# Performance work log

Hardware: AMD Instinct MI355X
Metric: run time of the kernel (lower is better)

## Reference

```python
import jax, jax.numpy as jnp
import numpy as np

# Config (mirrors HymbaLayer init + env constants)
DIM = 1024; NH = 16; NKV = 4; D = 64          # head_dim = DIM // NH
NATTN = NH // 2; NSSM = NH // 2; KVREP = NATTN // NKV
S = 16          # _HYMBA_SSM_STATE
NMETA = 4       # _HYMBA_META_TOK
BASE = 10000.0  # rope_base
CHUNK = 64      # _HYMBA_SCAN_CHUNK
B, T = 2, 2048


def _rms_norm(x, eps=1e-6):
    return x * jax.lax.rsqrt(jnp.mean(x * x, -1, keepdims=True) + eps)


def _rotary_cs(t_len, d, base):
    inv = 1.0 / (base ** (jnp.arange(0, d, 2, dtype=jnp.float32) / d))  # (d/2,)
    f = jnp.arange(t_len, dtype=jnp.float32)[:, None] * inv[None, :]    # (T, d/2)
    return jnp.cos(f), jnp.sin(f)


def _apply_rot(x, cos, sin):
    # x: (B, H, T, D); rotate-half style rotary
    d2 = x.shape[-1] // 2
    x1, x2 = x[..., :d2], x[..., d2:]
    c, s = cos[None, None], sin[None, None]
    return jnp.concatenate([x1 * c - x2 * s, x1 * s + x2 * c], -1)


def _scan_chunks(log_a, u, chunk):
    # Exact chunk-parallel diagonal scan: h_t = exp(log_a_t)*h_{t-1} + u_t
    b, t, s = u.shape
    nc = t // chunk
    la = log_a.reshape(b, nc, chunk, s)
    uu = u.reshape(b, nc, chunk, s)
    log_p = jnp.clip(jnp.cumsum(la, axis=2), -30.0, 0.0)
    p = jnp.exp(log_p)
    h_local = p * jnp.cumsum(uu * jnp.exp(-log_p), axis=2)

    def step(h0, args):
        hl, pc = args                          # (B, chunk, S)
        hc = hl + pc * h0[:, None, :]
        return hc[:, -1], hc

    _, hs = jax.lax.scan(step, jnp.zeros((b, s), u.dtype),
                         (jnp.swapaxes(h_local, 0, 1), jnp.swapaxes(p, 0, 1)))
    return jnp.swapaxes(hs, 0, 1).reshape(b, t, s)


def _mamba_head(logA, Bw, Cw, dtw, dtb, Ow, x):
    # x: (B, T, D); selective SSM with diagonal A
    dt = jnp.minimum(jax.nn.softplus(x @ dtw.T + dtb), 1.0)   # (B,T,S)
    A = jnp.minimum(-jnp.exp(logA), 10.0)                      # (S,)
    log_a = jnp.clip(dt * A, -0.5, 0.0)
    Bx = (x @ Bw.T) * dt
    Cc = x @ Cw.T
    h = _scan_chunks(log_a, Bx, CHUNK)                         # (B,T,S)
    y = jnp.sum(Cc * h, -1, keepdims=True)
    return h @ Ow.T + y * x[..., :1]


def _forward(x, meta_tokens, c_q_w, c_k_w, c_v_w, q_gain, ssm_in_w, proj_w,
             attn_scale, ssm_scale, ssm_logA, ssm_Bw, ssm_Cw, ssm_dtw, ssm_dtb, ssm_Ow):
    b, t, c = x.shape
    x_ext = jnp.concatenate([jnp.broadcast_to(meta_tokens, (b, NMETA, c)), x], 1)
    t_ext = t + NMETA
    q = (x_ext @ c_q_w.T).reshape(b, t_ext, NH, D).transpose(0, 2, 1, 3)
    k = (x_ext @ c_k_w.T).reshape(b, t_ext, NKV, D).transpose(0, 2, 1, 3)
    v = (x_ext @ c_v_w.T).reshape(b, t_ext, NKV, D).transpose(0, 2, 1, 3)
    q = _rms_norm(q); k = _rms_norm(k)
    cos, sin = _rotary_cs(t_ext, D, BASE)
    q = _apply_rot(q, cos, sin); k = _apply_rot(k, cos, sin)
    # GQA attention over the first NATTN heads, causal over T_ext
    q_attn = q[:, :NATTN] * q_gain[None, :, None, None]
    k_exp = jnp.repeat(k, KVREP, axis=1)
    v_exp = jnp.repeat(v, KVREP, axis=1)
    scores = jnp.einsum('bhqd,bhkd->bhqk', q_attn, k_exp) / jnp.sqrt(jnp.float32(D))
    mask = jnp.tril(jnp.ones((t_ext, t_ext), bool))
    scores = jnp.where(mask[None, None], scores, -jnp.inf)
    attn = jax.nn.softmax(scores, axis=-1)
    ao = jnp.einsum('bhqk,bhkd->bhqd', attn, v_exp)
    ao = ao[:, :, NMETA:].transpose(0, 2, 1, 3).reshape(b, t, NATTN * D) * attn_scale
    # SSM branch on the original (un-prepended) tokens
    ssm_x = (x @ ssm_in_w.T).reshape(b, t, NSSM, D)
    ssm_out = jax.vmap(_mamba_head, in_axes=(0, 0, 0, 0, 0, 0, 2), out_axes=2)(
        ssm_logA, ssm_Bw, ssm_Cw, ssm_dtw, ssm_dtb, ssm_Ow, ssm_x)
    ssm_out = ssm_out.reshape(b, t, NSSM * D) * ssm_scale
    return jnp.concatenate([ao, ssm_out], -1) @ proj_w.T


def setup_inputs() -> dict:
    key = jax.random.key(0)
    ks = jax.random.split(key, 16)
    r = lambda k, sh, sc=0.02: jax.random.normal(k, sh, jnp.float32) * sc
    return {
        'x': jax.random.normal(ks[0], (B, T, DIM), jnp.float32),
        'meta_tokens': r(ks[1], (1, NMETA, DIM)),
        'c_q_w': r(ks[2], (DIM, DIM)),
        'c_k_w': r(ks[3], (NKV * D, DIM)),
        'c_v_w': r(ks[4], (NKV * D, DIM)),
        'q_gain': jnp.full((NATTN,), 1.0, jnp.float32),
        'ssm_in_w': r(ks[5], (NSSM * D, DIM)),
        'proj_w': r(ks[6], (DIM, DIM)),
        'attn_scale': jnp.ones((1,), jnp.float32),
        'ssm_scale': jnp.ones((1,), jnp.float32),
        'ssm_logA': jax.random.normal(ks[7], (NSSM, S), jnp.float32) * 0.5,
        'ssm_Bw': r(ks[8], (NSSM, S, D), 0.05),
        'ssm_Cw': r(ks[9], (NSSM, S, D), 0.05),
        'ssm_dtw': r(ks[10], (NSSM, S, D), 0.05),
        'ssm_dtb': jnp.full((NSSM, S), -4.0, jnp.float32),
        'ssm_Ow': r(ks[11], (NSSM, D, S), 0.05),
    }


def reference(x, meta_tokens, c_q_w, c_k_w, c_v_w, q_gain, ssm_in_w, proj_w,
              attn_scale, ssm_scale, ssm_logA, ssm_Bw, ssm_Cw, ssm_dtw, ssm_dtb, ssm_Ow):
    return _forward(x, meta_tokens, c_q_w, c_k_w, c_v_w, q_gain, ssm_in_w, proj_w,
                    attn_scale, ssm_scale, ssm_logA, ssm_Bw, ssm_Cw, ssm_dtw, ssm_dtb, ssm_Ow)
```

## Files before the change

kernel.cpp:

```cpp
#include <hip/hip_runtime.h>
#include <hip/hip_bf16.h>
#include <math.h>

typedef __hip_bfloat16 bf16;
typedef __attribute__((ext_vector_type(8))) short short8;
typedef __attribute__((ext_vector_type(4))) float f32x4;

static constexpr int kB = 2;
static constexpr int kT = 2048;
static constexpr int kDIM = 1024;
static constexpr int kNMETA = 4;
static constexpr int kTEXT = kT + kNMETA;
static constexpr int kMEXT = kB * kTEXT;
static constexpr int kMPAD = 4224;
static constexpr int kMX = kB * kT;
static constexpr int kQT = 33;
static constexpr int kTP = 2112;

static constexpr size_t oXE = 0;
static constexpr size_t oYB = 0;
static constexpr size_t oLU = 8650752;
static constexpr size_t oCC = oLU + (size_t)kMX * 128 * 8;
static constexpr size_t oHL = oCC + (size_t)kMX * 128 * 4;
static constexpr size_t oX0 = oHL + (size_t)kMX * 128 * 2;
static constexpr size_t oQP = oX0 + (size_t)kMX * 8 * 4;
static constexpr size_t oKP = oQP + (size_t)kB * 8 * kTP * 64 * 2;
static constexpr size_t oVT = oKP + (size_t)kB * 4 * kTP * 64 * 2;
static constexpr size_t oWP = oVT + (size_t)kB * 4 * 64 * kTP * 2;
static constexpr size_t oWQ = oWP + (size_t)1024 * 1024 * 2;
static constexpr size_t oAO = 134217728;
static constexpr size_t oAL = oAO + (size_t)3 * kB * 8 * kTP * 64 * 4;

#define GLD_LDS16(gp, lp)                                                          \
  __builtin_amdgcn_global_load_lds((const __attribute__((address_space(1))) void*)(gp), \
                                   (__attribute__((address_space(3))) void*)(lp), 16, 0, 0)

__device__ __forceinline__ short bf2s(float f) {
  union { bf16 h; short s; } u;
  u.h = __float2bfloat16(f);
  return u.s;
}

__device__ __forceinline__ uint4 pack8(float4 a, float4 b) {
  union { bf16 h[8]; uint4 v; } u;
  u.h[0] = __float2bfloat16(a.x); u.h[1] = __float2bfloat16(a.y);
  u.h[2] = __float2bfloat16(a.z); u.h[3] = __float2bfloat16(a.w);
  u.h[4] = __float2bfloat16(b.x); u.h[5] = __float2bfloat16(b.y);
  u.h[6] = __float2bfloat16(b.z); u.h[7] = __float2bfloat16(b.w);
  return u.v;
}

__global__ __launch_bounds__(256) void prep_all(const float* __restrict__ cq, const float* __restrict__ ck,
                                                const float* __restrict__ cv, const float* __restrict__ sw,
                                                const float* __restrict__ pw,
                                                const float* __restrict__ x, const float* __restrict__ meta,
                                                bf16* __restrict__ wqkvsx, bf16* __restrict__ wproj,
                                                bf16* __restrict__ xe,
                                                bf16* __restrict__ Qp, bf16* __restrict__ Kp,
                                                bf16* __restrict__ Vt) {
  int i = blockIdx.x * 256 + threadIdx.x;
  if (i < 327680) {
    int row = i >> 7, v = i & 127;
    const float* src; bf16* dst;
    if (row < 512)       { src = cq + (size_t)row * 1024;          dst = wqkvsx + (size_t)row * 1024; }
    else if (row < 768)  { src = ck + (size_t)(row - 512) * 1024;  dst = wqkvsx + (size_t)row * 1024; }
    else if (row < 1024) { src = cv + (size_t)(row - 768) * 1024;  dst = wqkvsx + (size_t)row * 1024; }
    else if (row < 1536) { src = sw + (size_t)(row - 1024) * 1024; dst = wqkvsx + (size_t)row * 1024; }
    else                 { src = pw + (size_t)(row - 1536) * 1024; dst = wproj + (size_t)(row - 1536) * 1024; }
    float4 a0 = ((const float4*)src)[v * 2], a1 = ((const float4*)src)[v * 2 + 1];
    ((uint4*)dst)[v] = pack8(a0, a1);
  } else if (i < 868352) {
    int j = i - 327680;
    int r = j >> 7, v = j & 127;
    uint4 val = {0u, 0u, 0u, 0u};
    if (r < kMEXT) {
      int b = r / kTEXT, te = r - b * kTEXT;
      const float* src = (te < kNMETA) ? (meta + (size_t)te * kDIM)
                                       : (x + ((size_t)b * kT + (te - kNMETA)) * kDIM);
      float4 a0 = ((const float4*)src)[v * 2];
      float4 a1 = ((const float4*)src)[v * 2 + 1];
      val = pack8(a0, a1);
    }
    ((uint4*)(xe + (size_t)r * kDIM))[v] = val;
  } else {
    int j = i - 868352;
    if (j < 30720) {
      int k = j & 31, te = (j >> 5) % 60, bh = j / (60 * 32);
      *(unsigned int*)(Qp + ((size_t)bh * kTP + 2052 + te) * 64 + k * 2) = 0u;
    } else if (j < 46080) {
      int jj = j - 30720;
      int k = jj & 31, te = (jj >> 5) % 60, bh = jj / (60 * 32);
      *(unsigned int*)(Kp + ((size_t)bh * kTP + 2052 + te) * 64 + k * 2) = 0u;
    } else if (j < 61440) {
      int jj = j - 46080;
      int k = jj % 30, rowd = jj / 30;
      *(unsigned int*)(Vt + (size_t)rowd * kTP + 2052 + k * 2) = 0u;
    }
  }
}

template <int MODE>
__global__ __launch_bounds__(256) void gemm_t(const bf16* __restrict__ A,
                                              const bf16* __restrict__ W,
                                              void* __restrict__ O0, void* __restrict__ O1,
                                              void* __restrict__ O2,
                                              const float* __restrict__ q_gain,
                                              const float* __restrict__ dtw, const float* __restrict__ dtb,
                                              const float* __restrict__ Bw, const float* __restrict__ Cw,
                                              const float* __restrict__ logA,
                                              float* __restrict__ LU, float* __restrict__ CC,
                                              float* __restrict__ X0) {
  constexpr int SMEM_SZ = (MODE == 0) ? 25344 : 24576;
  __shared__ char smem[SMEM_SZ];
  const int tid = threadIdx.x;
  const int wave = tid >> 6, lane = tid & 63;
  const int quad = lane >> 4, l16 = lane & 15;
  const int bm = blockIdx.y * 128, bn = blockIdx.x * 64;
  const bf16* ag0 = A + (size_t)(bm + (tid >> 2)) * 1024 + (tid & 3) * 8;
  const bf16* ag1 = A + (size_t)(bm + 64 + (tid >> 2)) * 1024 + (tid & 3) * 8;
  const bf16* bg0 = W + (size_t)(bn + (tid >> 2)) * 1024 + (tid & 3) * 8;
  char* a00 = smem + wave * 1024;
  char* a10 = smem + 4096 + wave * 1024;
  char* a01 = smem + 8192 + wave * 1024;
  char* a11 = smem + 12288 + wave * 1024;
  char* bs0 = smem + 16384 + wave * 1024;
  char* bs1 = smem + 20480 + wave * 1024;
  f32x4 acc[2][4] = {};
  for (int k0 = 0; k0 < 1024; k0 += 64) {
    __syncthreads();
    GLD_LDS16(ag0, a00);
    GLD_LDS16(ag0 + 32, a01);
    GLD_LDS16(ag1, a10);
    GLD_LDS16(ag1 + 32, a11);
    GLD_LDS16(bg0, bs0);
    GLD_LDS16(bg0 + 32, bs1);
    ag0 += 64; ag1 += 64; bg0 += 64;
    __syncthreads();
#pragma unroll
    for (int p = 0; p < 2; ++p) {
      short8 af[2], bfr[4];
#pragma unroll
      for (int mi = 0; mi < 2; ++mi)
        af[mi] = *(const short8*)(smem + p * 8192 +
                                  (size_t)(wave * 32 + mi * 16 + l16) * 64 + quad * 16);
#pragma unroll
      for (int ni = 0; ni < 4; ++ni)
        bfr[ni] = *(const short8*)(smem + 16384 + p * 4096 +
                                   (size_t)(ni * 16 + l16) * 64 + quad * 16);
#pragma unroll
      for (int mi = 0; mi < 2; ++mi)
#pragma unroll
        for (int ni = 0; ni < 4; ++ni)
          acc[mi][ni] = __builtin_amdgcn_mfma_f32_16x16x32_bf16(af[mi], bfr[ni], acc[mi][ni], 0, 0, 0);
    }
  }
  if constexpr (MODE == 2) {
#pragma unroll
    for (int mi = 0; mi < 2; ++mi)
#pragma unroll
      for (int ni = 0; ni < 4; ++ni) {
        int colg = bn + ni * 16 + l16;
#pragma unroll
        for (int r = 0; r < 4; ++r) {
          int row = bm + wave * 32 + mi * 16 + quad * 4 + r;
          ((float*)O0)[(size_t)row * 1024 + colg] = acc[mi][ni][r];
        }
      }
  } else {
    const int tile = blockIdx.x;
    if (tile < 16) {
      float gain = (tile < 8) ? q_gain[tile] * 0.125f : 1.f;
      float inv0 = exp2f(-13.287712379549449f * (float)l16 * (1.f / 32.f));
      float inv1 = exp2f(-13.287712379549449f * (float)(l16 + 16) * (1.f / 32.f));
#pragma unroll
      for (int mi = 0; mi < 2; ++mi) {
        int row0 = bm + wave * 32 + mi * 16 + quad * 4;
        if (row0 >= kMEXT) continue;
        int b = row0 >= kTEXT ? 1 : 0;
        int te0 = row0 - b * kTEXT;
        if (tile < 12) {
          float ss[4];
#pragma unroll
          for (int r = 0; r < 4; ++r) {
            float s = 0.f;
#pragma unroll
            for (int ni = 0; ni < 4; ++ni) s += acc[mi][ni][r] * acc[mi][ni][r];
#pragma unroll
            for (int off = 1; off < 16; off <<= 1) s += __shfl_xor(s, off, 64);
            ss[r] = s;
          }
          bf16* base = (tile < 8)
            ? (bf16*)O0 + (((size_t)(b * 8 + tile)) * kTP + te0) * 64 + l16
            : (bf16*)O1 + (((size_t)(b * 4 + tile - 8)) * kTP + te0) * 64 + l16;
#pragma unroll
          for (int r = 0; r < 4; ++r) {
            float rn = rsqrtf(ss[r] * (1.f / 64.f) + 1e-6f) * gain;
            float te = (float)(te0 + r);
            float a0 = te * inv0, a1 = te * inv1;
            float c0 = __cosf(a0), s0 = __sinf(a0);
            float c1 = __cosf(a1), s1 = __sinf(a1);
            float v0 = acc[mi][0][r] * rn, v1 = acc[mi][1][r] * rn;
            float v2 = acc[mi][2][r] * rn, v3 = acc[mi][3][r] * rn;
            bf16* dst = base + (size_t)r * 64;
            dst[0]  = __float2bfloat16(v0 * c0 - v2 * s0);
            dst[16] = __float2bfloat16(v1 * c1 - v3 * s1);
            dst[32] = __float2bfloat16(v0 * s0 + v2 * c0);
            dst[48] = __float2bfloat16(v1 * s1 + v3 * c1);
          }
        } else {
          int hv = tile - 12;
#pragma unroll
          for (int ni = 0; ni < 4; ++ni) {
            union { unsigned long long q; bf16 hh[4]; } pw;
#pragma unroll
            for (int r = 0; r < 4; ++r) pw.hh[r] = __float2bfloat16(acc[mi][ni][r]);
            *(unsigned long long*)((bf16*)O2 +
                (((size_t)(b * 4 + hv)) * 64 + ni * 16 + l16) * kTP + te0) = pw.q;
          }
        }
      }
    } else {
      const int hd = tile - 16;
      __syncthreads();
      short (*Xl)[72] = (short(*)[72])smem;
      short (*Wl)[72] = (short(*)[72])(smem + 18432);
#pragma unroll
      for (int mi = 0; mi < 2; ++mi) {
        if (l16 == 0) {
#pragma unroll
          for (int r = 0; r < 4; ++r) {
            int row = bm + wave * 32 + mi * 16 + quad * 4 + r;
            if (row < kMEXT) {
              int bb = row >= kTEXT ? 1 : 0;
              int te = row - bb * kTEXT;
              if (te >= kNMETA) X0[(size_t)(bb * kT + te - kNMETA) * 8 + hd] = acc[mi][0][r];
            }
          }
        }
      }
#pragma unroll
      for (int mi = 0; mi < 2; ++mi)
#pragma unroll
        for (int ni = 0; ni < 4; ++ni)
#pragma unroll
          for (int r = 0; r < 4; ++r)
            Xl[wave * 32 + mi * 16 + quad * 4 + r][ni * 16 + l16] = bf2s(acc[mi][ni][r]);
      for (int s2 = tid; s2 < 384; s2 += 256) {
        int row = s2 >> 3, v = s2 & 7;
        const float* src = (row < 16) ? dtw + ((size_t)(hd * 16 + row)) * 64
                         : (row < 32) ? Bw + ((size_t)(hd * 16 + row - 16)) * 64
                                      : Cw + ((size_t)(hd * 16 + row - 32)) * 64;
        float4 a0 = ((const float4*)src)[v * 2];
        float4 a1 = ((const float4*)src)[v * 2 + 1];
        *(uint4*)&Wl[row][v * 8] = pack8(a0, a1);
      }
      __syncthreads();
      f32x4 a3[2][3] = {};
#pragma unroll
      for (int mt = 0; mt < 2; ++mt) {
        short8 xa0 = *(const short8*)&Xl[wave * 32 + mt * 16 + l16][quad * 8];
        short8 xa1 = *(const short8*)&Xl[wave * 32 + mt * 16 + l16][32 + quad * 8];
#pragma unroll
        for (int nb = 0; nb < 3; ++nb) {
          short8 wb0 = *(const short8*)&Wl[nb * 16 + l16][quad * 8];
          a3[mt][nb] = __builtin_amdgcn_mfma_f32_16x16x32_bf16(xa0, wb0, a3[mt][nb], 0, 0, 0);
          short8 wb1 = *(const short8*)&Wl[nb * 16 + l16][32 + quad * 8];
          a3[mt][nb] = __builtin_amdgcn_mfma_f32_16x16x32_bf16(xa1, wb1, a3[mt][nb], 0, 0, 0);
        }
      }
      float dtb_v = dtb[hd * 16 + l16];
      float A_v = fminf(-expf(logA[hd * 16 + l16]), 10.f);
#pragma unroll
      for (int mt = 0; mt < 2; ++mt)
#pragma unroll
        for (int r = 0; r < 4; ++r) {
          int row = bm + wave * 32 + mt * 16 + quad * 4 + r;
          if (row >= kMEXT) continue;
          int bb = row >= kTEXT ? 1 : 0;
          int te = row - bb * kTEXT;
          if (te < kNMETA) continue;
          size_t ix = (size_t)(bb * kT + te - kNMETA) * 128 + hd * 16 + l16;
          float raw = a3[mt][0][r] + dtb_v;
          float sp = fmaxf(raw, 0.f) + log1pf(expf(-fabsf(raw)));
          float dt = fminf(sp, 1.f);
          float lav = fminf(fmaxf(dt * A_v, -0.5f), 0.f);
          *(float2*)(LU + 2 * ix) = make_float2(lav, a3[mt][1][r] * dt);
          CC[ix] = a3[mt][2][r];
        }
    }
  }
}

__global__ __launch_bounds__(256) void attn_part(const bf16* __restrict__ Qp,
                                                 const bf16* __restrict__ Kp,
                                                 const bf16* __restrict__ Vt,
                                                 float* __restrict__ AO, float* __restrict__ AL) {
  __shared__ short Ks[64][72];
  __shared__ short Vs[64][72];
  __shared__ short Ps[4][16][72];
  const int part = blockIdx.x % 3;
  const int qt = (kQT - 1) - (blockIdx.x / 3);
  const int h = blockIdx.y, b = blockIdx.z;
  const int kvh = h >> 1;
  const int tid = threadIdx.x, wave = tid >> 6, lane = tid & 63;
  const int quad = lane >> 4, l16 = lane & 15;
  const int ntiles = qt + 1;
  const int s1 = ntiles / 3, s2 = (2 * ntiles) / 3;
  const int kt_begin = (part == 0) ? 0 : (part == 1 ? s1 : s2);
  const int kt_end = (part == 0) ? s1 : (part == 1 ? s2 : ntiles);
  const int kt_pf = (kt_begin < kt_end) ? kt_begin : 0;

  short8 qf[2];
  {
    const bf16* qrow = Qp + (((size_t)(b * 8 + h)) * kTP + qt * 64 + wave * 16 + l16) * 64 + quad * 8;
    qf[0] = *(const short8*)(qrow);
    qf[1] = *(const short8*)(qrow + 32);
  }
  short8 ones;
#pragma unroll
  for (int i = 0; i < 8; ++i) ones[i] = (short)0x3F80;

  const bf16* kbase = Kp + ((size_t)(b * 4 + kvh)) * kTP * 64;
  const bf16* vbase = Vt + ((size_t)(b * 4 + kvh)) * 64 * kTP;

  const int r0row = tid >> 3, r0c8 = tid & 7;
  const int r1row = (256 + tid) >> 3, r1c8 = tid & 7;

  f32x4 O[4] = {};
  f32x4 lacc = {};
  const int q_abs = qt * 64 + wave * 16 + l16;

  uint4 kr0 = *(const uint4*)(kbase + (size_t)(kt_pf * 64 + r0row) * 64 + r0c8 * 8);
  uint4 kr1 = *(const uint4*)(kbase + (size_t)(kt_pf * 64 + r1row) * 64 + r1c8 * 8);
  uint4 vr0 = *(const uint4*)(vbase + (size_t)r0row * kTP + kt_pf * 64 + r0c8 * 8);
  uint4 vr1 = *(const uint4*)(vbase + (size_t)r1row * kTP + kt_pf * 64 + r1c8 * 8);

  for (int kt = kt_begin; kt < kt_end; ++kt) {
    __syncthreads();
    *(uint4*)&Ks[r0row][r0c8 * 8] = kr0;
    *(uint4*)&Ks[r1row][r1c8 * 8] = kr1;
    *(uint4*)&Vs[r0row][r0c8 * 8] = vr0;
    *(uint4*)&Vs[r1row][r1c8 * 8] = vr1;
    if (kt + 1 < kt_end) {
      int kn = (kt + 1) * 64;
      kr0 = *(const uint4*)(kbase + (size_t)(kn + r0row) * 64 + r0c8 * 8);
      kr1 = *(const uint4*)(kbase + (size_t)(kn + r1row) * 64 + r1c8 * 8);
      vr0 = *(const uint4*)(vbase + (size_t)r0row * kTP + kn + r0c8 * 8);
      vr1 = *(const uint4*)(vbase + (size_t)r1row * kTP + kn + r1c8 * 8);
    }
    __syncthreads();

    f32x4 st[4] = {};
#pragma unroll
    for (int nb = 0; nb < 4; ++nb) {
      short8 ak0 = *(const short8*)&Ks[nb * 16 + l16][quad * 8];
      st[nb] = __builtin_amdgcn_mfma_f32_16x16x32_bf16(ak0, qf[0], st[nb], 0, 0, 0);
      short8 ak1 = *(const short8*)&Ks[nb * 16 + l16][32 + quad * 8];
      st[nb] = __builtin_amdgcn_mfma_f32_16x16x32_bf16(ak1, qf[1], st[nb], 0, 0, 0);
    }
    if (kt == qt) {
      int key0 = kt * 64 + quad * 4;
#pragma unroll
      for (int nb = 0; nb < 4; ++nb)
#pragma unroll
        for (int rg = 0; rg < 4; ++rg)
          if (key0 + nb * 16 + rg > q_abs) st[nb][rg] = -1e30f;
    }
#pragma unroll
    for (int nb = 0; nb < 4; ++nb) {
      union { unsigned long long q; bf16 hh[4]; } pw;
#pragma unroll
      for (int rg = 0; rg < 4; ++rg) pw.hh[rg] = __float2bfloat16(__expf(st[nb][rg]));
      *(unsigned long long*)&Ps[wave][l16][nb * 16 + quad * 4] = pw.q;
    }
    short8 pf0 = *(const short8*)&Ps[wave][l16][quad * 8];
    short8 pf1 = *(const short8*)&Ps[wave][l16][32 + quad * 8];
    lacc = __builtin_amdgcn_mfma_f32_16x16x32_bf16(pf0, ones, lacc, 0, 0, 0);
    lacc = __builtin_amdgcn_mfma_f32_16x16x32_bf16(pf1, ones, lacc, 0, 0, 0);
#pragma unroll
    for (int db = 0; db < 4; ++db) {
      short8 bv0 = *(const short8*)&Vs[db * 16 + l16][quad * 8];
      O[db] = __builtin_amdgcn_mfma_f32_16x16x32_bf16(pf0, bv0, O[db], 0, 0, 0);
      short8 bv1 = *(const short8*)&Vs[db * 16 + l16][32 + quad * 8];
      O[db] = __builtin_amdgcn_mfma_f32_16x16x32_bf16(pf1, bv1, O[db], 0, 0, 0);
    }
  }
  size_t hb = (((size_t)part * 2 + b) * 8 + h);
  float* aoB = AO + hb * kTP * 64;
  float* alB = AL + hb * kTP;
#pragma unroll
  for (int rg = 0; rg < 4; ++rg) {
    int q = qt * 64 + wave * 16 + quad * 4 + rg;
    float* dst = aoB + (size_t)q * 64 + l16;
#pragma unroll
    for (int db = 0; db < 4; ++db) dst[db * 16] = O[db][rg];
    if (l16 == 0) alB[q] = lacc[rg];
  }
}

__global__ __launch_bounds__(256) void ssm_scan(const float* __restrict__ LU, bf16* __restrict__ HL) {
  __shared__ float sH[4][64], sP[4][64], sH0[4][64];
  const int tid = threadIdx.x;
  const int ch = tid & 3, c = tid >> 2;
  const int chain = blockIdx.x * 4 + ch;
  const int b = chain >> 7, hs = chain & 127;
  const float2* LU2 = (const float2*)LU;
  const size_t base = ((size_t)b * kT) * 128 + hs;
  float H = 0.f, cum = 0.f;
  for (int i = 0; i < 32; ++i) {
    float2 lu = LU2[base + (size_t)(c * 32 + i) * 128];
    cum += lu.x;
    H = __expf(lu.x) * H + lu.y;
  }
  sH[ch][c] = H;
  sP[ch][c] = __expf(cum);
  __syncthreads();
  const int wv = tid >> 6, lane = tid & 63;
  float Hs = sH[wv][lane], Ps = sP[wv][lane];
#pragma unroll
  for (int off = 1; off < 64; off <<= 1) {
    float Hp = __shfl_up(Hs, off, 64);
    float Pp = __shfl_up(Ps, off, 64);
    if (lane >= off) { Hs = Hs + Ps * Hp; Ps = Ps * Pp; }
  }
  float Hex = __shfl_up(Hs, 1, 64);
  if (lane == 0) Hex = 0.f;
  sH0[wv][lane] = Hex;
  __syncthreads();
  float h = sH0[ch][c];
  for (int i = 0; i < 32; ++i) {
    size_t ix = base + (size_t)(c * 32 + i) * 128;
    float2 lu = LU2[ix];
    h = __expf(lu.x) * h + lu.y;
    HL[ix] = __float2bfloat16(h);
  }
}

__global__ __launch_bounds__(256) void combine_out(const float* __restrict__ AO,
                                                   const float* __restrict__ AL,
                                                   const float* __restrict__ attn_scale,
                                                   const bf16* __restrict__ HL, const float* __restrict__ CC,
                                                   const float* __restrict__ X0, const float* __restrict__ Ow,
                                                   const float* __restrict__ ssm_scale,
                                                   bf16* __restrict__ Y) {
  if (blockIdx.x < 528) {
    int id = blockIdx.x * 256 + threadIdx.x;
    int d16 = id & 3;
    int tmp = id >> 2;
    int q = tmp % kTP; tmp /= kTP;
    int h = tmp & 7, b = tmp >> 3;
    if (q < kNMETA || q >= kTEXT) return;
    size_t hb0 = ((size_t)b * 8 + h), hb1 = ((size_t)(2 + b) * 8 + h), hb2 = ((size_t)(4 + b) * 8 + h);
    float l = AL[hb0 * kTP + q] + AL[hb1 * kTP + q] + AL[hb2 * kTP + q];
    float so = attn_scale[0] / fmaxf(l, 1e-30f);
    const float4* p0 = (const float4*)(AO + (hb0 * kTP + q) * 64 + d16 * 16);
    const float4* p1 = (const float4*)(AO + (hb1 * kTP + q) * 64 + d16 * 16);
    const float4* p2 = (const float4*)(AO + (hb2 * kTP + q) * 64 + d16 * 16);
    bf16* dst = Y + ((size_t)(b * kT + q - kNMETA)) * kDIM + h * 64 + d16 * 16;
#pragma unroll
    for (int i = 0; i < 4; ++i) {
      float4 a = p0[i], c = p1[i], e = p2[i];
      dst[i * 4 + 0] = __float2bfloat16((a.x + c.x + e.x) * so);
      dst[i * 4 + 1] = __float2bfloat16((a.y + c.y + e.y) * so);
      dst[i * 4 + 2] = __float2bfloat16((a.z + c.z + e.z) * so);
      dst[i * 4 + 3] = __float2bfloat16((a.w + c.w + e.w) * so);
    }
  } else {
    int id = (blockIdx.x - 528) * 256 + threadIdx.x;
    int d4 = id & 3, h = (id >> 2) & 7, t = (id >> 5) & 2047, b = id >> 16;
    size_t ix0 = ((size_t)(b * kT + t)) * 128 + h * 16;
    float hv[16], y = 0.f;
#pragma unroll
    for (int s = 0; s < 16; ++s) {
      float v = __bfloat162float(HL[ix0 + s]);
      hv[s] = v;
      y += CC[ix0 + s] * v;
    }
    float x0 = X0[(size_t)(b * kT + t) * 8 + h];
    float scl = ssm_scale[0];
    const float* ow = Ow + ((size_t)h * 64 + d4 * 16) * 16;
    bf16* dst = Y + ((size_t)(b * kT + t)) * kDIM + 512 + h * 64 + d4 * 16;
    float yx = y * x0;
#pragma unroll
    for (int d = 0; d < 16; ++d) {
      float acc = yx;
      const float* owr = ow + d * 16;
#pragma unroll
      for (int s = 0; s < 16; ++s) acc += hv[s] * owr[s];
      dst[d] = __float2bfloat16(acc * scl);
    }
  }
}

extern "C" void kernel_launch(void* const* d_in, const int* in_sizes, int n_in,
                              void* d_out, int out_size, void* d_ws, size_t ws_size,
                              hipStream_t stream) {
  (void)in_sizes; (void)n_in; (void)out_size; (void)ws_size;
  const float* x        = (const float*)d_in[0];
  const float* meta     = (const float*)d_in[1];
  const float* c_q_w    = (const float*)d_in[2];
  const float* c_k_w    = (const float*)d_in[3];
  const float* c_v_w    = (const float*)d_in[4];
  const float* q_gain   = (const float*)d_in[5];
  const float* ssm_in_w = (const float*)d_in[6];
  const float* proj_w   = (const float*)d_in[7];
  const float* attn_sc  = (const float*)d_in[8];
  const float* ssm_sc   = (const float*)d_in[9];
  const float* ssm_logA = (const float*)d_in[10];
  const float* ssm_Bw   = (const float*)d_in[11];
  const float* ssm_Cw   = (const float*)d_in[12];
  const float* ssm_dtw  = (const float*)d_in[13];
  const float* ssm_dtb  = (const float*)d_in[14];
  const float* ssm_Ow   = (const float*)d_in[15];

  char* w = (char*)d_ws;
  bf16*  XE = (bf16*)(w + oXE);
  bf16*  YB = (bf16*)(w + oYB);
  bf16*  QP = (bf16*)(w + oQP);
  bf16*  KP = (bf16*)(w + oKP);
  bf16*  VT = (bf16*)(w + oVT);
  bf16*  WQ = (bf16*)(w + oWQ);
  bf16*  WP = (bf16*)(w + oWP);
  float* LU = (float*)(w + oLU);
  float* CC = (float*)(w + oCC);
  bf16*  HL = (bf16*)(w + oHL);
  float* X0 = (float*)(w + oX0);
  float* AO = (float*)(w + oAO);
  float* AL = (float*)(w + oAL);

  prep_all<<<3632, 256, 0, stream>>>(c_q_w, c_k_w, c_v_w, ssm_in_w, proj_w,
                                     x, meta, WQ, WP, XE, QP, KP, VT);

  gemm_t<0><<<dim3(24, kMPAD / 128), 256, 0, stream>>>(XE, WQ, QP, KP, VT, q_gain,
                                                       ssm_dtw, ssm_dtb, ssm_Bw, ssm_Cw,
                                                       ssm_logA, LU, CC, X0);

  attn_part<<<dim3(kQT * 3, 8, kB), 256, 0, stream>>>(QP, KP, VT, AO, AL);

  ssm_scan<<<64, 256, 0, stream>>>(LU, HL);

  combine_out<<<1040, 256, 0, stream>>>(AO, AL, attn_sc, HL, CC, X0, ssm_Ow, ssm_sc, YB);

  gemm_t<2><<<dim3(16, kMX / 128), 256, 0, stream>>>(YB, WP, d_out, nullptr, nullptr, nullptr,
                                                     nullptr, nullptr, nullptr, nullptr, nullptr,
                                                     nullptr, nullptr, nullptr);
}
```

Before: 213.8 us.

## Double-buffer GEMM LDS tiles and merge SSM scan into attention launch

The shared GEMM kernel now uses two LDS buffers. The next K-slice is issued with the global-to-LDS loads while MFMAs run on the current slice, which removes one barrier per iteration and overlaps memory with compute. Separately, the SSM scan kernel is folded into the attention kernel as 64 extra leading blocks. This removes a launch and lets the scan run alongside the attention blocks. The cost is doubled LDS per GEMM block (48 KB), which may cut GEMM occupancy.

```diff
diff --git a/kernel.cpp b/kernel.cpp
--- a/kernel.cpp
+++ b/kernel.cpp
@@ -110,8 +110,7 @@
                                               const float* __restrict__ logA,
                                               float* __restrict__ LU, float* __restrict__ CC,
                                               float* __restrict__ X0) {
-  constexpr int SMEM_SZ = (MODE == 0) ? 25344 : 24576;
-  __shared__ char smem[SMEM_SZ];
+  __shared__ char smem[49152];
   const int tid = threadIdx.x;
   const int wave = tid >> 6, lane = tid & 63;
   const int quad = lane >> 4, l16 = lane & 15;
@@ -119,33 +118,41 @@
   const bf16* ag0 = A + (size_t)(bm + (tid >> 2)) * 1024 + (tid & 3) * 8;
   const bf16* ag1 = A + (size_t)(bm + 64 + (tid >> 2)) * 1024 + (tid & 3) * 8;
   const bf16* bg0 = W + (size_t)(bn + (tid >> 2)) * 1024 + (tid & 3) * 8;
-  char* a00 = smem + wave * 1024;
-  char* a10 = smem + 4096 + wave * 1024;
-  char* a01 = smem + 8192 + wave * 1024;
-  char* a11 = smem + 12288 + wave * 1024;
-  char* bs0 = smem + 16384 + wave * 1024;
-  char* bs1 = smem + 20480 + wave * 1024;
   f32x4 acc[2][4] = {};
-  for (int k0 = 0; k0 < 1024; k0 += 64) {
+  {
+    char* sb = smem + wave * 1024;
+    GLD_LDS16(ag0, sb);
+    GLD_LDS16(ag1, sb + 4096);
+    GLD_LDS16(ag0 + 32, sb + 8192);
+    GLD_LDS16(ag1 + 32, sb + 12288);
+    GLD_LDS16(bg0, sb + 16384);
+    GLD_LDS16(bg0 + 32, sb + 20480);
+    ag0 += 64; ag1 += 64; bg0 += 64;
+  }
+  for (int k = 0; k < 16; ++k) {
+    char* cur = smem + (k & 1) * 24576;
+    char* nxt = smem + ((k & 1) ^ 1) * 24576;
     __syncthreads();
-    GLD_LDS16(ag0, a00);
-    GLD_LDS16(ag0 + 32, a01);
-    GLD_LDS16(ag1, a10);
-    GLD_LDS16(ag1 + 32, a11);
-    GLD_LDS16(bg0, bs0);
-    GLD_LDS16(bg0 + 32, bs1);
-    ag0 += 64; ag1 += 64; bg0 += 64;
-    __syncthreads();
+    if (k < 15) {
+      char* sb = nxt + wave * 1024;
+      GLD_LDS16(ag0, sb);
+      GLD_LDS16(ag1, sb + 4096);
+      GLD_LDS16(ag0 + 32, sb + 8192);
+      GLD_LDS16(ag1 + 32, sb + 12288);
+      GLD_LDS16(bg0, sb + 16384);
+      GLD_LDS16(bg0 + 32, sb + 20480);
+      ag0 += 64; ag1 += 64; bg0 += 64;
+    }
 #pragma unroll
     for (int p = 0; p < 2; ++p) {
       short8 af[2], bfr[4];
 #pragma unroll
       for (int mi = 0; mi < 2; ++mi)
-        af[mi] = *(const short8*)(smem + p * 8192 +
+        af[mi] = *(const short8*)(cur + p * 8192 +
                                   (size_t)(wave * 32 + mi * 16 + l16) * 64 + quad * 16);
 #pragma unroll
       for (int ni = 0; ni < 4; ++ni)
-        bfr[ni] = *(const short8*)(smem + 16384 + p * 4096 +
+        bfr[ni] = *(const short8*)(cur + 16384 + p * 4096 +
                                    (size_t)(ni * 16 + l16) * 64 + quad * 16);
 #pragma unroll
       for (int mi = 0; mi < 2; ++mi)
@@ -291,16 +298,60 @@
   }
 }
 
-__global__ __launch_bounds__(256) void attn_part(const bf16* __restrict__ Qp,
+__global__ __launch_bounds__(256) void attn_scan(const bf16* __restrict__ Qp,
                                                  const bf16* __restrict__ Kp,
                                                  const bf16* __restrict__ Vt,
-                                                 float* __restrict__ AO, float* __restrict__ AL) {
-  __shared__ short Ks[64][72];
-  __shared__ short Vs[64][72];
-  __shared__ short Ps[4][16][72];
-  const int part = blockIdx.x % 3;
-  const int qt = (kQT - 1) - (blockIdx.x / 3);
-  const int h = blockIdx.y, b = blockIdx.z;
+                                                 float* __restrict__ AO, float* __restrict__ AL,
+                                                 const float* __restrict__ LU, bf16* __restrict__ HL) {
+  __shared__ char sraw[27648];
+  if (blockIdx.x < 64) {
+    float (*sH)[64] = (float(*)[64])sraw;
+    float (*sP)[64] = (float(*)[64])(sraw + 1024);
+    float (*sH0)[64] = (float(*)[64])(sraw + 2048);
+    const int tid = threadIdx.x;
+    const int ch = tid & 3, c = tid >> 2;
+    const int chain = blockIdx.x * 4 + ch;
+    const int b = chain >> 7, hs = chain & 127;
+    const float2* LU2 = (const float2*)LU;
+    const size_t base = ((size_t)b * kT) * 128 + hs;
+    float H = 0.f, cum = 0.f;
+    for (int i = 0; i < 32; ++i) {
+      float2 lu = LU2[base + (size_t)(c * 32 + i) * 128];
+      cum += lu.x;
+      H = __expf(lu.x) * H + lu.y;
+    }
+    sH[ch][c] = H;
+    sP[ch][c] = __expf(cum);
+    __syncthreads();
+    const int wv = tid >> 6, lane = tid & 63;
+    float Hs = sH[wv][lane], Ps = sP[wv][lane];
+#pragma unroll
+    for (int off = 1; off < 64; off <<= 1) {
+      float Hp = __shfl_up(Hs, off, 64);
+      float Pp = __shfl_up(Ps, off, 64);
+      if (lane >= off) { Hs = Hs + Ps * Hp; Ps = Ps * Pp; }
+    }
+    float Hex = __shfl_up(Hs, 1, 64);
+    if (lane == 0) Hex = 0.f;
+    sH0[wv][lane] = Hex;
+    __syncthreads();
+    float h = sH0[ch][c];
+    for (int i = 0; i < 32; ++i) {
+      size_t ix = base + (size_t)(c * 32 + i) * 128;
+      float2 lu = LU2[ix];
+      h = __expf(lu.x) * h + lu.y;
+      HL[ix] = __float2bfloat16(h);
+    }
+    return;
+  }
+  short (*Ks)[72] = (short(*)[72])sraw;
+  short (*Vs)[72] = (short(*)[72])(sraw + 9216);
+  short (*Ps)[16][72] = (short(*)[16][72])(sraw + 18432);
+  const int i = blockIdx.x - 64;
+  const int xq = i % 99;
+  const int h = (i / 99) & 7, b = i / 792;
+  const int part = xq % 3;
+  const int qt = (kQT - 1) - (xq / 3);
   const int kvh = h >> 1;
   const int tid = threadIdx.x, wave = tid >> 6, lane = tid & 63;
   const int quad = lane >> 4, l16 = lane & 15;
@@ -318,7 +369,7 @@
   }
   short8 ones;
 #pragma unroll
-  for (int i = 0; i < 8; ++i) ones[i] = (short)0x3F80;
+  for (int j = 0; j < 8; ++j) ones[j] = (short)0x3F80;
 
   const bf16* kbase = Kp + ((size_t)(b * 4 + kvh)) * kTP * 64;
   const bf16* vbase = Vt + ((size_t)(b * 4 + kvh)) * 64 * kTP;
@@ -395,44 +446,6 @@
 #pragma unroll
     for (int db = 0; db < 4; ++db) dst[db * 16] = O[db][rg];
     if (l16 == 0) alB[q] = lacc[rg];
-  }
-}
-
-__global__ __launch_bounds__(256) void ssm_scan(const float* __restrict__ LU, bf16* __restrict__ HL) {
-  __shared__ float sH[4][64], sP[4][64], sH0[4][64];
-  const int tid = threadIdx.x;
-  const int ch = tid & 3, c = tid >> 2;
-  const int chain = blockIdx.x * 4 + ch;
-  const int b = chain >> 7, hs = chain & 127;
-  const float2* LU2 = (const float2*)LU;
-  const size_t base = ((size_t)b * kT) * 128 + hs;
-  float H = 0.f, cum = 0.f;
-  for (int i = 0; i < 32; ++i) {
-    float2 lu = LU2[base + (size_t)(c * 32 + i) * 128];
-    cum += lu.x;
-    H = __expf(lu.x) * H + lu.y;
-  }
-  sH[ch][c] = H;
-  sP[ch][c] = __expf(cum);
-  __syncthreads();
-  const int wv = tid >> 6, lane = tid & 63;
-  float Hs = sH[wv][lane], Ps = sP[wv][lane];
-#pragma unroll
-  for (int off = 1; off < 64; off <<= 1) {
-    float Hp = __shfl_up(Hs, off, 64);
-    float Pp = __shfl_up(Ps, off, 64);
-    if (lane >= off) { Hs = Hs + Ps * Hp; Ps = Ps * Pp; }
-  }
-  float Hex = __shfl_up(Hs, 1, 64);
-  if (lane == 0) Hex = 0.f;
-  sH0[wv][lane] = Hex;
-  __syncthreads();
-  float h = sH0[ch][c];
-  for (int i = 0; i < 32; ++i) {
-    size_t ix = base + (size_t)(c * 32 + i) * 128;
-    float2 lu = LU2[ix];
-    h = __expf(lu.x) * h + lu.y;
-    HL[ix] = __float2bfloat16(h);
   }
 }
 
@@ -458,12 +471,12 @@
     const float4* p2 = (const float4*)(AO + (hb2 * kTP + q) * 64 + d16 * 16);
     bf16* dst = Y + ((size_t)(b * kT + q - kNMETA)) * kDIM + h * 64 + d16 * 16;
 #pragma unroll
-    for (int i = 0; i < 4; ++i) {
-      float4 a = p0[i], c = p1[i], e = p2[i];
-      dst[i * 4 + 0] = __float2bfloat16((a.x + c.x + e.x) * so);
-      dst[i * 4 + 1] = __float2bfloat16((a.y + c.y + e.y) * so);
-      dst[i * 4 + 2] = __float2bfloat16((a.z + c.z + e.z) * so);
-      dst[i * 4 + 3] = __float2bfloat16((a.w + c.w + e.w) * so);
+    for (int j = 0; j < 4; ++j) {
+      float4 a = p0[j], c = p1[j], e = p2[j];
+      dst[j * 4 + 0] = __float2bfloat16((a.x + c.x + e.x) * so);
+      dst[j * 4 + 1] = __float2bfloat16((a.y + c.y + e.y) * so);
+      dst[j * 4 + 2] = __float2bfloat16((a.z + c.z + e.z) * so);
+      dst[j * 4 + 3] = __float2bfloat16((a.w + c.w + e.w) * so);
     }
   } else {
     int id = (blockIdx.x - 528) * 256 + threadIdx.x;
@@ -535,9 +548,7 @@
                                                        ssm_dtw, ssm_dtb, ssm_Bw, ssm_Cw,
                                                        ssm_logA, LU, CC, X0);
 
-  attn_part<<<dim3(kQT * 3, 8, kB), 256, 0, stream>>>(QP, KP, VT, AO, AL);
-
-  ssm_scan<<<64, 256, 0, stream>>>(LU, HL);
+  attn_scan<<<64 + kQT * 3 * 8 * kB, 256, 0, stream>>>(QP, KP, VT, AO, AL, LU, HL);
 
   combine_out<<<1040, 256, 0, stream>>>(AO, AL, attn_sc, HL, CC, X0, ssm_Ow, ssm_sc, YB);
 
```

Result: faster. 198.2 us (-7.3%).
